# Optimization experiments

Hardware: AMD Instinct MI355X
Metric: run time of the kernel (lower is better)

## Reference

```python
import jax, jax.numpy as jnp
import numpy as np

F_DIM = 128
N_RBF = 20
CUTOFF = 5.0
N_LAYERS = 3
EPS = 1e-8


def setup_inputs() -> dict:
    key = jax.random.key(0)
    ks = jax.random.split(key, 16)
    N, E = 10000, 320000
    atomic_numbers = jax.random.randint(ks[0], (N,), 0, 100)
    r_ij = jax.random.normal(ks[1], (E, 3), dtype=jnp.float32)
    idx_i = jnp.sort(jax.random.randint(ks[2], (E,), 0, N))
    idx_j = jax.random.randint(ks[3], (E,), 0, N)
    emb = jax.random.normal(ks[4], (100, F_DIM), dtype=jnp.float32)
    emb = emb.at[0].set(0.0)  # padding_idx=0
    s = 0.05
    return {
        "atomic_numbers": atomic_numbers,
        "r_ij": r_ij,
        "idx_i": idx_i,
        "idx_j": idx_j,
        "embedding": emb,
        "filt_W": jax.random.normal(ks[5], (N_RBF, N_LAYERS * 3 * F_DIM), dtype=jnp.float32) * s,
        "filt_b": jax.random.normal(ks[6], (N_LAYERS * 3 * F_DIM,), dtype=jnp.float32) * s,
        "int_W1": jax.random.normal(ks[7], (N_LAYERS, F_DIM, F_DIM), dtype=jnp.float32) * s,
        "int_b1": jax.random.normal(ks[8], (N_LAYERS, F_DIM), dtype=jnp.float32) * s,
        "int_W2": jax.random.normal(ks[9], (N_LAYERS, F_DIM, 3 * F_DIM), dtype=jnp.float32) * s,
        "int_b2": jax.random.normal(ks[10], (N_LAYERS, 3 * F_DIM), dtype=jnp.float32) * s,
        "mix_W1": jax.random.normal(ks[11], (N_LAYERS, 2 * F_DIM, F_DIM), dtype=jnp.float32) * s,
        "mix_b1": jax.random.normal(ks[12], (N_LAYERS, F_DIM), dtype=jnp.float32) * s,
        "mix_W2": jax.random.normal(ks[13], (N_LAYERS, F_DIM, 3 * F_DIM), dtype=jnp.float32) * s,
        "mix_b2": jax.random.normal(ks[14], (N_LAYERS, 3 * F_DIM), dtype=jnp.float32) * s,
        "mux_W": jax.random.normal(ks[15], (N_LAYERS, F_DIM, 2 * F_DIM), dtype=jnp.float32) * s,
    }


def _painn(embedding, filt_W, filt_b, int_W1, int_b1, int_W2, int_b2,
           mix_W1, mix_b1, mix_W2, mix_b2, mux_W,
           r_ij, atomic_numbers, idx_i, idx_j):
    N = atomic_numbers.shape[0]
    F = F_DIM
    d_ij = jnp.linalg.norm(r_ij, axis=1, keepdims=True)          # [E,1]
    dir_ij = r_ij / d_ij                                          # [E,3]
    # Gaussian RBF expansion
    offset = jnp.linspace(0.0, CUTOFF, N_RBF, dtype=jnp.float32)
    coeff = -0.5 / (offset[1] - offset[0]) ** 2
    phi = jnp.exp(coeff * (d_ij[..., None] - offset) ** 2)        # [E,1,n_rbf]
    # Cosine cutoff
    fcut = 0.5 * (jnp.cos(d_ij * jnp.pi / CUTOFF) + 1.0) * (d_ij < CUTOFF)  # [E,1]
    filters = (phi @ filt_W + filt_b) * fcut[..., None]           # [E,1,L*3F]
    filter_list = jnp.split(filters, N_LAYERS, axis=-1)

    q = embedding[atomic_numbers][:, None, :]                     # [N,1,F]
    mu = jnp.zeros((N, 3, F), dtype=q.dtype)

    for i in range(N_LAYERS):
        Wij = filter_list[i]                                      # [E,1,3F]
        # interaction
        h = jax.nn.silu(q @ int_W1[i] + int_b1[i])
        x = h @ int_W2[i] + int_b2[i]                             # [N,1,3F]
        xj = x[idx_j]                                             # [E,1,3F]
        muj = mu[idx_j]                                           # [E,3,F]
        xw = Wij * xj
        dq, dmuR, dmumu = jnp.split(xw, 3, axis=-1)               # each [E,1,F]
        dq = jax.ops.segment_sum(dq, idx_i, num_segments=N)       # [N,1,F]
        dmu = dmuR * dir_ij[:, :, None] + dmumu * muj             # [E,3,F]
        dmu = jax.ops.segment_sum(dmu, idx_i, num_segments=N)     # [N,3,F]
        q = q + dq
        mu = mu + dmu
        # mixing
        mu_mix = mu @ mux_W[i]                                    # [N,3,2F]
        mu_V, mu_W = jnp.split(mu_mix, 2, axis=-1)
        mu_Vn = jnp.sqrt(jnp.sum(mu_V ** 2, axis=-2, keepdims=True) + EPS)  # [N,1,F]
        ctx = jnp.concatenate([q, mu_Vn], axis=-1)                # [N,1,2F]
        h = jax.nn.silu(ctx @ mix_W1[i] + mix_b1[i])
        x = h @ mix_W2[i] + mix_b2[i]                             # [N,1,3F]
        dq_i, dmu_i, dqmu_i = jnp.split(x, 3, axis=-1)
        dmu_i = dmu_i * mu_W                                      # [N,3,F]
        dqmu_i = dqmu_i * jnp.sum(mu_V * mu_W, axis=1, keepdims=True)
        q = q + dq_i + dqmu_i
        mu = mu + dmu_i
    return q[:, 0, :], mu


def reference(atomic_numbers, r_ij, idx_i, idx_j, embedding, filt_W, filt_b,
              int_W1, int_b1, int_W2, int_b2, mix_W1, mix_b1, mix_W2, mix_b2, mux_W):
    return _painn(embedding, filt_W, filt_b, int_W1, int_b1, int_W2, int_b2,
                  mix_W1, mix_b1, mix_W2, mix_b2, mux_W,
                  r_ij, atomic_numbers, idx_i, idx_j)
```

## Files before the change

kernel.cpp:

```cpp
#include <hip/hip_runtime.h>
#include <hip/hip_bf16.h>
#include <hip/hip_fp16.h>

#define F_DIM 128
#define N_RBF 20
#define CUTOFF 5.0f
#define PI_F 3.14159265358979323846f
#define NPB 4

typedef float v2f __attribute__((ext_vector_type(2)));
typedef __attribute__((ext_vector_type(8))) short bf16x8;
typedef __attribute__((ext_vector_type(4))) float f32x4;
typedef _Float16 h2f __attribute__((ext_vector_type(2)));

__device__ __forceinline__ unsigned int bf16_rtne(float f) {
    unsigned int u = __float_as_uint(f);
    u += 0x7fffu + ((u >> 16) & 1u);
    return u >> 16;
}
__device__ __forceinline__ unsigned int pack_bf2(float lo, float hi) {
    return bf16_rtne(lo) | (bf16_rtne(hi) << 16);
}
__device__ __forceinline__ float unpk_lo(unsigned int u) {
    return __uint_as_float(u << 16);
}
__device__ __forceinline__ float unpk_hi(unsigned int u) {
    return __uint_as_float(u & 0xffff0000u);
}
__device__ __forceinline__ float bf16_to_f(unsigned short s) {
    return __uint_as_float(((unsigned int)s) << 16);
}
__device__ __forceinline__ unsigned int pack_h2(float lo, float hi) {
    h2f h = (h2f){(_Float16)lo, (_Float16)hi};
    return __builtin_bit_cast(unsigned int, h);
}
__device__ __forceinline__ float fdot2f(unsigned int a, unsigned int b, float c) {
    h2f ha = __builtin_bit_cast(h2f, a);
    h2f hb = __builtin_bit_cast(h2f, b);
#if __has_builtin(__builtin_amdgcn_fdot2)
    return __builtin_amdgcn_fdot2(ha, hb, c, false);
#else
    return c + (float)ha.x * (float)hb.x + (float)ha.y * (float)hb.y;
#endif
}

__global__ __launch_bounds__(256) void k_rowptr(const int* __restrict__ idx_i,
                                                int* __restrict__ row_ptr, int N, int E) {
    int i = blockIdx.x * blockDim.x + threadIdx.x;
    if (i > N) return;
    if (i == N) { row_ptr[N] = E; return; }
    int lo = 0, hi = E;
    while (lo < hi) {
        int mid = (lo + hi) >> 1;
        if (idx_i[mid] < i) lo = mid + 1; else hi = mid;
    }
    row_ptr[i] = lo;
}

__global__ __launch_bounds__(256) void k_init(const int* __restrict__ Z,
                                              const float* __restrict__ emb,
                                              float* __restrict__ q,
                                              unsigned int* __restrict__ P,
                                              float* __restrict__ muD, int N) {
    int idx = blockIdx.x * blockDim.x + threadIdx.x;
    if (idx < N * F_DIM) {
        int n = idx >> 7, f = idx & 127;
        q[idx] = emb[Z[n] * F_DIM + f];
    }
    if (idx < N * 384) { P[idx] = 0u; muD[idx] = 0.f; }
}

__global__ __launch_bounds__(256) void k_prep(const float* __restrict__ muxW,
                                              const float* __restrict__ W1,
                                              const float* __restrict__ W2,
                                              const float* __restrict__ iW1,
                                              const float* __restrict__ iW2,
                                              const float* __restrict__ filt_W,
                                              unsigned short* __restrict__ muxWt,
                                              unsigned short* __restrict__ W1t,
                                              unsigned short* __restrict__ W2t,
                                              unsigned short* __restrict__ iW1t,
                                              unsigned short* __restrict__ iW2t,
                                              unsigned int* __restrict__ filtWh) {
    int idx = blockIdx.x * 256 + threadIdx.x;
    if (idx < 98304) {
        int l = idx / 32768, rem = idx % 32768;
        int c = rem / 128, k = rem % 128;
        muxWt[idx] = (unsigned short)bf16_rtne(muxW[l * 32768 + k * 256 + c]);
    } else if (idx < 196608) {
        int i2 = idx - 98304;
        int l = i2 / 32768, rem = i2 % 32768;
        int c = rem / 256, k = rem % 256;
        W1t[i2] = (unsigned short)bf16_rtne(W1[l * 32768 + k * 128 + c]);
    } else if (idx < 344064) {
        int i2 = idx - 196608;
        int l = i2 / 49152, rem = i2 % 49152;
        int c = rem / 128, k = rem % 128;
        W2t[i2] = (unsigned short)bf16_rtne(W2[l * 49152 + k * 384 + c]);
    } else if (idx < 393216) {
        int i2 = idx - 344064;
        int l = i2 / 16384, rem = i2 % 16384;
        int c = rem / 128, k = rem % 128;
        iW1t[i2] = (unsigned short)bf16_rtne(iW1[l * 16384 + k * 128 + c]);
    } else if (idx < 540672) {
        int i2 = idx - 393216;
        int l = i2 / 49152, rem = i2 % 49152;
        int c = rem / 128, k = rem % 128;
        iW2t[i2] = (unsigned short)bf16_rtne(iW2[l * 49152 + k * 384 + c]);
    } else if (idx < 552192) {
        int i2 = idx - 540672;
        int l = i2 / 3840, rem = i2 % 3840;
        int kp = rem / 384, c = rem % 384;
        float lo = filt_W[(2 * kp) * 1152 + l * 384 + c];
        float hi = filt_W[(2 * kp + 1) * 1152 + l * 384 + c];
        filtWh[i2] = pack_h2(lo, hi);
    }
}

__global__ __launch_bounds__(256) void k_geom(const float* __restrict__ r,
                                              unsigned int* __restrict__ geom, int E) {
    int e = blockIdx.x * blockDim.x + threadIdx.x;
    if (e >= E) return;
    float x = r[e * 3], y = r[e * 3 + 1], z = r[e * 3 + 2];
    float d = sqrtf(x * x + y * y + z * z);
    float inv = 1.f / d;
    float fc = (d < CUTOFF) ? 0.5f * (__cosf(d * (PI_F / CUTOFF)) + 1.f) : 0.f;
    unsigned int* g = geom + (size_t)e * 16;
    g[0] = __float_as_uint(x * inv);
    g[1] = __float_as_uint(y * inv);
    g[2] = __float_as_uint(z * inv);
    g[3] = __float_as_uint(fc);
    const float delta = CUTOFF / (N_RBF - 1);
    const float coeff = -0.5f / (delta * delta);
    float ph[N_RBF];
#pragma unroll
    for (int k = 0; k < N_RBF; k++) {
        float t = d - k * delta;
        ph[k] = __expf(coeff * t * t) * fc;
    }
#pragma unroll
    for (int k = 0; k < N_RBF / 2; k++)
        g[4 + k] = pack_h2(ph[2 * k], ph[2 * k + 1]);
}

__global__ __launch_bounds__(256) void k_node_mfma(
        const float* __restrict__ q,
        const unsigned short* __restrict__ iW1t,
        const float* __restrict__ b1,
        const unsigned short* __restrict__ iW2t,
        const float* __restrict__ b2,
        unsigned int* __restrict__ P, int N) {
    __shared__ unsigned short A[16 * 136];
    __shared__ unsigned short Ah[16 * 136];
    __shared__ float Xs[16 * 396];
    int t = threadIdx.x;
    int w = t >> 6, l = t & 63, quad = l >> 4, c0 = l & 15;
    int n0 = blockIdx.x * 16;

#pragma unroll
    for (int i = 0; i < 4; i++) {
        int flat = i * 256 + t;
        int node = flat >> 6, cp = flat & 63;
        int gn = n0 + node;
        unsigned int v = 0u;
        if (gn < N) { const float* s = q + (size_t)gn * 128 + 2 * cp; v = pack_bf2(s[0], s[1]); }
        *(unsigned int*)&A[node * 136 + 2 * cp] = v;
    }
    __syncthreads();

    bf16x8 a1[4];
#pragma unroll
    for (int ks = 0; ks < 4; ks++)
        a1[ks] = *(const bf16x8*)&A[c0 * 136 + ks * 32 + quad * 8];
#pragma unroll
    for (int jj = 0; jj < 2; jj++) {
        int jg = 2 * w + jj;
        float bb = b1[16 * jg + c0];
        f32x4 acc = (f32x4){bb, bb, bb, bb};
#pragma unroll
        for (int ks = 0; ks < 4; ks++) {
            bf16x8 b = *(const bf16x8*)&iW1t[(16 * jg + c0) * 128 + ks * 32 + quad * 8];
            acc = __builtin_amdgcn_mfma_f32_16x16x32_bf16(a1[ks], b, acc, 0, 0, 0);
        }
#pragma unroll
        for (int r = 0; r < 4; r++) {
            float aa = acc[r];
            Ah[(quad * 4 + r) * 136 + 16 * jg + c0] =
                (unsigned short)bf16_rtne(aa / (1.f + __expf(-aa)));
        }
    }
    __syncthreads();

    bf16x8 a3[4];
#pragma unroll
    for (int ks = 0; ks < 4; ks++)
        a3[ks] = *(const bf16x8*)&Ah[c0 * 136 + ks * 32 + quad * 8];
#pragma unroll
    for (int jj = 0; jj < 6; jj++) {
        int jx = 6 * w + jj;
        float bb = b2[16 * jx + c0];
        f32x4 acc = (f32x4){bb, bb, bb, bb};
#pragma unroll
        for (int ks = 0; ks < 4; ks++) {
            bf16x8 b = *(const bf16x8*)&iW2t[(16 * jx + c0) * 128 + ks * 32 + quad * 8];
            acc = __builtin_amdgcn_mfma_f32_16x16x32_bf16(a3[ks], b, acc, 0, 0, 0);
        }
#pragma unroll
        for (int r = 0; r < 4; r++)
            Xs[(quad * 4 + r) * 396 + 16 * jx + c0] = acc[r];
    }
    __syncthreads();

    int n = t >> 4, fi = (t & 15) * 8;
    int gn = n0 + n;
    if (gn < N) {
        size_t base = (size_t)gn * 384;
        unsigned int d[8];
#pragma unroll
        for (int k = 0; k < 8; k++) {
            float x0 = Xs[n * 396 + fi + k];
            float x1 = Xs[n * 396 + 128 + fi + k];
            float x2 = Xs[n * 396 + 256 + fi + k];
            d[k] = pack_bf2(x0, x1);
            ((unsigned short*)&P[base + 256 + fi + k])[0] = (unsigned short)bf16_rtne(x2);
        }
        *(uint4*)&P[base + fi]     = make_uint4(d[0], d[1], d[2], d[3]);
        *(uint4*)&P[base + fi + 4] = make_uint4(d[4], d[5], d[6], d[7]);
    }
}

template <bool HAS_MU>
__global__ __launch_bounds__(256) void k_edge(
        const unsigned int* __restrict__ P,
        const unsigned int* __restrict__ geom,
        const int* __restrict__ idx_j,
        const int* __restrict__ row_ptr,
        const unsigned int* __restrict__ filtWh,
        const float* __restrict__ filt_b,
        int layer,
        float* __restrict__ q,
        float* __restrict__ muD, int N) {
    __shared__ float red[4][128];
    int t = threadIdx.x;
    int f = t & 127;
    int sub = __builtin_amdgcn_readfirstlane(t >> 7);

    unsigned int Wq[N_RBF / 2], Wr[N_RBF / 2], Wm[N_RBF / 2];
    const unsigned int* Fh = filtWh + layer * 3840;
#pragma unroll
    for (int j = 0; j < N_RBF / 2; j++) {
        Wq[j] = Fh[j * 384 + f];
        Wr[j] = Fh[j * 384 + 128 + f];
        Wm[j] = Fh[j * 384 + 256 + f];
    }
    float bf0 = filt_b[layer * 384 + f];
    float bf1 = filt_b[layer * 384 + 128 + f];
    float bf2 = filt_b[layer * 384 + 256 + f];

    int i0 = blockIdx.x * NPB;
    for (int nn = 0; nn < NPB; nn++) {
        int i = i0 + nn;
        if (i >= N) break;
        int rs = __builtin_amdgcn_readfirstlane(row_ptr[i]);
        int re = __builtin_amdgcn_readfirstlane(row_ptr[i + 1]);
        float dq = 0.f;
        v2f dm01 = (v2f){0.f, 0.f};
        float dm2 = 0.f;

        for (int e = rs + sub; e < re; e += 2) {
            int j = __builtin_amdgcn_readfirstlane(idx_j[e]);
            const unsigned int* Pj = P + (size_t)j * 384;
            unsigned int A = Pj[f];
            unsigned int B = 0, C = 0;
            if (HAS_MU) { B = Pj[128 + f]; C = Pj[256 + f]; }

            const unsigned int* g = geom + (size_t)e * 16;
            float dirx = __uint_as_float(g[0]);
            float diry = __uint_as_float(g[1]);
            float dirz = __uint_as_float(g[2]);
            float fcv  = __uint_as_float(g[3]);
            unsigned int pp[10];
#pragma unroll
            for (int k = 0; k < 10; k++) pp[k] = g[4 + k];

            float wq = fcv * bf0, wr = fcv * bf1, wm = fcv * bf2;
#pragma unroll
            for (int k = 0; k < N_RBF / 2; k++) {
                wq = fdot2f(pp[k], Wq[k], wq);
                wr = fdot2f(pp[k], Wr[k], wr);
                if (HAS_MU) wm = fdot2f(pp[k], Wm[k], wm);
            }

            float xq = unpk_lo(A), xr = unpk_hi(A);
            dq += wq * xq;
            float s_r = wr * xr;
            if (HAS_MU) {
                float xm = unpk_lo(C);
                float s_m = wm * xm;
                dm01 += (v2f){s_r, s_r} * (v2f){dirx, diry} +
                        (v2f){s_m, s_m} * (v2f){unpk_lo(B), unpk_hi(B)};
                dm2  += s_r * dirz + s_m * unpk_hi(C);
            } else {
                dm01 += (v2f){s_r, s_r} * (v2f){dirx, diry};
                dm2  += s_r * dirz;
            }
        }

        if (sub == 1) { red[0][f] = dq; red[1][f] = dm01.x; red[2][f] = dm01.y; red[3][f] = dm2; }
        __syncthreads();
        if (sub == 0) {
            dq += red[0][f];
            float d0 = dm01.x + red[1][f], d1 = dm01.y + red[2][f];
            dm2 += red[3][f];
            q[(size_t)i * 128 + f] += dq;
            size_t base = (size_t)i * 384;
            if (HAS_MU) {
                muD[base + f]       += d0;
                muD[base + 128 + f] += d1;
                muD[base + 256 + f] += dm2;
            } else {
                muD[base + f]       = d0;
                muD[base + 128 + f] = d1;
                muD[base + 256 + f] = dm2;
            }
        }
        __syncthreads();
    }
}

__global__ __launch_bounds__(256) void k_mix_fused(
        float* __restrict__ q, float* __restrict__ mu,
        const unsigned short* __restrict__ muxWt,
        const unsigned short* __restrict__ W1t,
        const unsigned short* __restrict__ W2t,
        const float* __restrict__ b1,
        const float* __restrict__ b2,
        const unsigned short* __restrict__ niW1t,
        const float* __restrict__ nib1,
        const unsigned short* __restrict__ niW2t,
        const float* __restrict__ nib2,
        int has_node,
        unsigned int* __restrict__ P, int N) {
    __shared__ unsigned short A[16 * 264];
    __shared__ unsigned short Wsp[3 * 16 * 136];
    __shared__ float Xs[16 * 396];
    __shared__ float Ss[16 * 140];
    int t = threadIdx.x;
    int w = t >> 6, l = t & 63, quad = l >> 4, c0 = l & 15;
    int n0 = blockIdx.x * 16;

#pragma unroll
    for (int i = 0; i < 4; i++) {
        int flat = i * 256 + t;
        int node = flat >> 6, cp = flat & 63;
        int gn = n0 + node;
        unsigned int v = 0u;
        if (gn < N) { const float* s = q + (size_t)gn * 128 + 2 * cp; v = pack_bf2(s[0], s[1]); }
        *(unsigned int*)&A[node * 264 + 2 * cp] = v;
    }

    f32x4 vn2[2], S[2];
#pragma unroll
    for (int jj = 0; jj < 2; jj++) { vn2[jj] = (f32x4){0,0,0,0}; S[jj] = (f32x4){0,0,0,0}; }

    for (int c = 0; c < 3; c++) {
#pragma unroll
        for (int i = 0; i < 4; i++) {
            int flat = i * 256 + t;
            int node = flat >> 6, cp = flat & 63;
            int gn = n0 + node;
            unsigned int v = 0u;
            if (gn < N) {
                const float* s = mu + (size_t)gn * 384 + c * 128 + 2 * cp;
                v = pack_bf2(s[0], s[1]);
            }
            *(unsigned int*)&A[node * 264 + 128 + 2 * cp] = v;
        }
        __syncthreads();
        bf16x8 af[4];
#pragma unroll
        for (int ks = 0; ks < 4; ks++)
            af[ks] = *(const bf16x8*)&A[c0 * 264 + 128 + ks * 32 + quad * 8];
#pragma unroll
        for (int jj = 0; jj < 2; jj++) {
            int jv = 2 * w + jj;
            f32x4 V = (f32x4){0,0,0,0}, Wm = (f32x4){0,0,0,0};
#pragma unroll
            for (int ks = 0; ks < 4; ks++) {
                bf16x8 bV = *(const bf16x8*)&muxWt[(16 * jv + c0) * 128 + ks * 32 + quad * 8];
                V = __builtin_amdgcn_mfma_f32_16x16x32_bf16(af[ks], bV, V, 0, 0, 0);
            }
#pragma unroll
            for (int ks = 0; ks < 4; ks++) {
                bf16x8 bW = *(const bf16x8*)&muxWt[(16 * (jv + 8) + c0) * 128 + ks * 32 + quad * 8];
                Wm = __builtin_amdgcn_mfma_f32_16x16x32_bf16(af[ks], bW, Wm, 0, 0, 0);
            }
            vn2[jj] += V * V;
            S[jj]   += V * Wm;
#pragma unroll
            for (int r = 0; r < 4; r++)
                Wsp[c * 2176 + (quad * 4 + r) * 136 + 16 * jv + c0] =
                    (unsigned short)bf16_rtne(Wm[r]);
        }
        __syncthreads();
    }

#pragma unroll
    for (int jj = 0; jj < 2; jj++) {
        int jv = 2 * w + jj;
#pragma unroll
        for (int r = 0; r < 4; r++)
            A[(quad * 4 + r) * 264 + 128 + 16 * jv + c0] =
                (unsigned short)bf16_rtne(sqrtf(vn2[jj][r] + 1e-8f));
    }
    __syncthreads();

    bf16x8 a2[8];
#pragma unroll
    for (int ks = 0; ks < 8; ks++)
        a2[ks] = *(const bf16x8*)&A[c0 * 264 + ks * 32 + quad * 8];
    {
        unsigned short htmp[2][4];
#pragma unroll
        for (int jj = 0; jj < 2; jj++) {
            int jg = 2 * w + jj;
            float bb = b1[16 * jg + c0];
            f32x4 acc = (f32x4){bb, bb, bb, bb};
#pragma unroll
            for (int ks = 0; ks < 8; ks++) {
                bf16x8 b = *(const bf16x8*)&W1t[(16 * jg + c0) * 256 + ks * 32 + quad * 8];
                acc = __builtin_amdgcn_mfma_f32_16x16x32_bf16(a2[ks], b, acc, 0, 0, 0);
            }
#pragma unroll
            for (int r = 0; r < 4; r++) {
                float aa = acc[r];
                htmp[jj][r] = (unsigned short)bf16_rtne(aa / (1.f + __expf(-aa)));
            }
        }
        __syncthreads();
#pragma unroll
        for (int jj = 0; jj < 2; jj++) {
            int jg = 2 * w + jj;
#pragma unroll
            for (int r = 0; r < 4; r++)
                A[(quad * 4 + r) * 264 + 128 + 16 * jg + c0] = htmp[jj][r];
        }
    }
    __syncthreads();

    bf16x8 a3[4];
#pragma unroll
    for (int ks = 0; ks < 4; ks++)
        a3[ks] = *(const bf16x8*)&A[c0 * 264 + 128 + ks * 32 + quad * 8];
#pragma unroll
    for (int jj = 0; jj < 6; jj++) {
        int jx = 6 * w + jj;
        float bb = b2[16 * jx + c0];
        f32x4 acc = (f32x4){bb, bb, bb, bb};
#pragma unroll
        for (int ks = 0; ks < 4; ks++) {
            bf16x8 b = *(const bf16x8*)&W2t[(16 * jx + c0) * 128 + ks * 32 + quad * 8];
            acc = __builtin_amdgcn_mfma_f32_16x16x32_bf16(a3[ks], b, acc, 0, 0, 0);
        }
#pragma unroll
        for (int r = 0; r < 4; r++)
            Xs[(quad * 4 + r) * 396 + 16 * jx + c0] = acc[r];
    }
#pragma unroll
    for (int jj = 0; jj < 2; jj++) {
        int jv = 2 * w + jj;
#pragma unroll
        for (int r = 0; r < 4; r++)
            Ss[(quad * 4 + r) * 140 + 16 * jv + c0] = S[jj][r];
    }
    __syncthreads();

    int n = t >> 4, fi = (t & 15) * 8;
    int gn = n0 + n;
    if (gn < N) {
        float* qp = q + (size_t)gn * 128 + fi;
        float qn[8];
#pragma unroll
        for (int k = 0; k < 8; k++) {
            qn[k] = qp[k] + Xs[n * 396 + fi + k] +
                    Xs[n * 396 + 256 + fi + k] * Ss[n * 140 + fi + k];
            qp[k] = qn[k];
        }
        unsigned int qd[4];
#pragma unroll
        for (int p = 0; p < 4; p++) qd[p] = pack_bf2(qn[2 * p], qn[2 * p + 1]);
        *(uint4*)&A[n * 264 + fi] = make_uint4(qd[0], qd[1], qd[2], qd[3]);

        size_t base = (size_t)gn * 384;
        float m[3][8];
#pragma unroll
        for (int c = 0; c < 3; c++) {
            float* mp = mu + base + c * 128 + fi;
#pragma unroll
            for (int k = 0; k < 8; k++) {
                m[c][k] = mp[k] + Xs[n * 396 + 128 + fi + k] *
                                  bf16_to_f(Wsp[c * 2176 + n * 136 + fi + k]);
                mp[k] = m[c][k];
            }
        }
        unsigned int d[8];
#pragma unroll
        for (int k = 0; k < 8; k++) {
            d[k] = pack_bf2(m[0][k], m[1][k]);
            ((unsigned short*)&P[base + 256 + fi + k])[1] = (unsigned short)bf16_rtne(m[2][k]);
        }
        *(uint4*)&P[base + 128 + fi]     = make_uint4(d[0], d[1], d[2], d[3]);
        *(uint4*)&P[base + 128 + fi + 4] = make_uint4(d[4], d[5], d[6], d[7]);
    }
    __syncthreads();

    if (has_node) {
        unsigned short* Ah = Wsp;
        bf16x8 a1[4];
#pragma unroll
        for (int ks = 0; ks < 4; ks++)
            a1[ks] = *(const bf16x8*)&A[c0 * 264 + ks * 32 + quad * 8];
#pragma unroll
        for (int jj = 0; jj < 2; jj++) {
            int jg = 2 * w + jj;
            float bb = nib1[16 * jg + c0];
            f32x4 acc = (f32x4){bb, bb, bb, bb};
#pragma unroll
            for (int ks = 0; ks < 4; ks++) {
                bf16x8 b = *(const bf16x8*)&niW1t[(16 * jg + c0) * 128 + ks * 32 + quad * 8];
                acc = __builtin_amdgcn_mfma_f32_16x16x32_bf16(a1[ks], b, acc, 0, 0, 0);
            }
#pragma unroll
            for (int r = 0; r < 4; r++) {
                float aa = acc[r];
                Ah[(quad * 4 + r) * 136 + 16 * jg + c0] =
                    (unsigned short)bf16_rtne(aa / (1.f + __expf(-aa)));
            }
        }
        __syncthreads();

        bf16x8 a4[4];
#pragma unroll
        for (int ks = 0; ks < 4; ks++)
            a4[ks] = *(const bf16x8*)&Ah[c0 * 136 + ks * 32 + quad * 8];
#pragma unroll
        for (int jj = 0; jj < 6; jj++) {
            int jx = 6 * w + jj;
            float bb = nib2[16 * jx + c0];
            f32x4 acc = (f32x4){bb, bb, bb, bb};
#pragma unroll
            for (int ks = 0; ks < 4; ks++) {
                bf16x8 b = *(const bf16x8*)&niW2t[(16 * jx + c0) * 128 + ks * 32 + quad * 8];
                acc = __builtin_amdgcn_mfma_f32_16x16x32_bf16(a4[ks], b, acc, 0, 0, 0);
            }
#pragma unroll
            for (int r = 0; r < 4; r++)
                Xs[(quad * 4 + r) * 396 + 16 * jx + c0] = acc[r];
        }
        __syncthreads();

        if (gn < N) {
            size_t base = (size_t)gn * 384;
            unsigned int d[8];
#pragma unroll
            for (int k = 0; k < 8; k++) {
                float x0 = Xs[n * 396 + fi + k];
                float x1 = Xs[n * 396 + 128 + fi + k];
                float x2 = Xs[n * 396 + 256 + fi + k];
                d[k] = pack_bf2(x0, x1);
                ((unsigned short*)&P[base + 256 + fi + k])[0] = (unsigned short)bf16_rtne(x2);
            }
            *(uint4*)&P[base + fi]     = make_uint4(d[0], d[1], d[2], d[3]);
            *(uint4*)&P[base + fi + 4] = make_uint4(d[4], d[5], d[6], d[7]);
        }
    }
}

extern "C" void kernel_launch(void* const* d_in, const int* in_sizes, int n_in,
                              void* d_out, int out_size, void* d_ws, size_t ws_size,
                              hipStream_t stream) {
    const int*   Z      = (const int*)d_in[0];
    const float* r_ij   = (const float*)d_in[1];
    const int*   idx_i  = (const int*)d_in[2];
    const int*   idx_j  = (const int*)d_in[3];
    const float* emb    = (const float*)d_in[4];
    const float* filt_W = (const float*)d_in[5];
    const float* filt_b = (const float*)d_in[6];
    const float* int_W1 = (const float*)d_in[7];
    const float* int_b1 = (const float*)d_in[8];
    const float* int_W2 = (const float*)d_in[9];
    const float* int_b2 = (const float*)d_in[10];
    const float* mix_W1 = (const float*)d_in[11];
    const float* mix_b1 = (const float*)d_in[12];
    const float* mix_W2 = (const float*)d_in[13];
    const float* mix_b2 = (const float*)d_in[14];
    const float* mux_W  = (const float*)d_in[15];

    int N = in_sizes[0];
    int E = in_sizes[2];

    float* q   = (float*)d_out;
    float* muD = q + (size_t)N * 128;

    unsigned int* geom = (unsigned int*)d_ws;
    unsigned int* P = geom + (size_t)E * 16;
    int* row_ptr = (int*)(P + (size_t)N * 384);
    uintptr_t waddr = (uintptr_t)(row_ptr + N + 1);
    waddr = (waddr + 15) & ~(uintptr_t)15;
    unsigned short* muxWt = (unsigned short*)waddr;
    unsigned short* W1t   = muxWt + 98304;
    unsigned short* W2t   = W1t + 98304;
    unsigned short* iW1t  = W2t + 147456;
    unsigned short* iW2t  = iW1t + 49152;
    unsigned int* filtWh  = (unsigned int*)(iW2t + 147456);

    k_rowptr<<<(N + 1 + 255) / 256, 256, 0, stream>>>(idx_i, row_ptr, N, E);
    k_init<<<((size_t)N * 384 + 255) / 256, 256, 0, stream>>>(Z, emb, q, P, muD, N);
    k_geom<<<(E + 255) / 256, 256, 0, stream>>>(r_ij, geom, E);
    k_prep<<<2157, 256, 0, stream>>>(mux_W, mix_W1, mix_W2, int_W1, int_W2, filt_W,
                                     muxWt, W1t, W2t, iW1t, iW2t, filtWh);

    int tiles = (N + 15) / 16;
    k_node_mfma<<<tiles, 256, 0, stream>>>(
        q, iW1t, int_b1, iW2t, int_b2, P, N);
    for (int l = 0; l < 3; l++) {
        if (l == 0)
            k_edge<false><<<(N + NPB - 1) / NPB, 256, 0, stream>>>(
                P, geom, idx_j, row_ptr, filtWh, filt_b, l, q, muD, N);
        else
            k_edge<true><<<(N + NPB - 1) / NPB, 256, 0, stream>>>(
                P, geom, idx_j, row_ptr, filtWh, filt_b, l, q, muD, N);
        int nl = (l < 2) ? (l + 1) : 0;
        k_mix_fused<<<tiles, 256, 0, stream>>>(
            q, muD, muxWt + (size_t)l * 32768, W1t + (size_t)l * 32768,
            W2t + (size_t)l * 49152, mix_b1 + l * 128, mix_b2 + l * 384,
            iW1t + (size_t)nl * 16384, int_b1 + nl * 128,
            iW2t + (size_t)nl * 49152, int_b2 + nl * 384,
            (l < 2) ? 1 : 0, P, N);
    }
}
```

Baseline: 543.2 us.

## Compute edge filter weights with fp16 MFMA tiles staged through shared memory

Replaces the per-thread fdot2 RBF-to-filter projection in the edge kernel with 16x16x32 fp16 MFMA over tiles of 16 edges. The bias is folded in as an extra K column multiplied by fc. Filter weights are re-laid out in prep as K-padded fp16 B fragments, and the resulting per-edge weights go into an LDS buffer that the gather loop then reads. This cuts redundant ALU work, since the old code recomputed each edge's filter per feature lane. In exchange it adds two block syncs per 16-edge tile, and rows have only about 32 edges, so padded tiles waste work.

```diff
diff --git a/kernel.cpp b/kernel.cpp
--- a/kernel.cpp
+++ b/kernel.cpp
@@ -12,6 +12,7 @@
 typedef __attribute__((ext_vector_type(8))) short bf16x8;
 typedef __attribute__((ext_vector_type(4))) float f32x4;
 typedef _Float16 h2f __attribute__((ext_vector_type(2)));
+typedef _Float16 f16x8 __attribute__((ext_vector_type(8)));
 
 __device__ __forceinline__ unsigned int bf16_rtne(float f) {
     unsigned int u = __float_as_uint(f);
@@ -33,15 +34,6 @@
 __device__ __forceinline__ unsigned int pack_h2(float lo, float hi) {
     h2f h = (h2f){(_Float16)lo, (_Float16)hi};
     return __builtin_bit_cast(unsigned int, h);
-}
-__device__ __forceinline__ float fdot2f(unsigned int a, unsigned int b, float c) {
-    h2f ha = __builtin_bit_cast(h2f, a);
-    h2f hb = __builtin_bit_cast(h2f, b);
-#if __has_builtin(__builtin_amdgcn_fdot2)
-    return __builtin_amdgcn_fdot2(ha, hb, c, false);
-#else
-    return c + (float)ha.x * (float)hb.x + (float)ha.y * (float)hb.y;
-#endif
 }
 
 __global__ __launch_bounds__(256) void k_rowptr(const int* __restrict__ idx_i,
@@ -76,12 +68,13 @@
                                               const float* __restrict__ iW1,
                                               const float* __restrict__ iW2,
                                               const float* __restrict__ filt_W,
+                                              const float* __restrict__ filt_b,
                                               unsigned short* __restrict__ muxWt,
                                               unsigned short* __restrict__ W1t,
                                               unsigned short* __restrict__ W2t,
                                               unsigned short* __restrict__ iW1t,
                                               unsigned short* __restrict__ iW2t,
-                                              unsigned int* __restrict__ filtWh) {
+                                              unsigned short* __restrict__ filtWt) {
     int idx = blockIdx.x * 256 + threadIdx.x;
     if (idx < 98304) {
         int l = idx / 32768, rem = idx % 32768;
@@ -107,13 +100,15 @@
         int l = i2 / 49152, rem = i2 % 49152;
         int c = rem / 128, k = rem % 128;
         iW2t[i2] = (unsigned short)bf16_rtne(iW2[l * 49152 + k * 384 + c]);
-    } else if (idx < 552192) {
+    } else if (idx < 568320) {
         int i2 = idx - 540672;
-        int l = i2 / 3840, rem = i2 % 3840;
-        int kp = rem / 384, c = rem % 384;
-        float lo = filt_W[(2 * kp) * 1152 + l * 384 + c];
-        float hi = filt_W[(2 * kp + 1) * 1152 + l * 384 + c];
-        filtWh[i2] = pack_h2(lo, hi);
+        int l = i2 / 9216, rem = i2 % 9216;
+        int c = rem / 24, k = rem % 24;
+        float v = 0.f;
+        if (k < 20)       v = filt_W[k * 1152 + l * 384 + c];
+        else if (k == 20) v = filt_b[l * 384 + c];
+        _Float16 hv = (_Float16)v;
+        filtWt[i2] = __builtin_bit_cast(unsigned short, hv);
     }
 }
 
@@ -141,6 +136,8 @@
 #pragma unroll
     for (int k = 0; k < N_RBF / 2; k++)
         g[4 + k] = pack_h2(ph[2 * k], ph[2 * k + 1]);
+    g[14] = pack_h2(fc, 0.f);
+    g[15] = 0u;
 }
 
 __global__ __launch_bounds__(256) void k_node_mfma(
@@ -229,33 +226,43 @@
     }
 }
 
+__device__ __forceinline__ f16x8 load_phi_frag(const unsigned int* __restrict__ geom,
+                                               int ts, int c0, int quad, int E) {
+    int ea = ts + c0;
+    if (ea >= E) ea = E - 1;
+    f16x8 a = {};
+    if (quad < 3)
+        a = *(const f16x8*)&geom[(size_t)ea * 16 + 4 + quad * 4];
+    return a;
+}
+
 template <bool HAS_MU>
 __global__ __launch_bounds__(256) void k_edge(
         const unsigned int* __restrict__ P,
         const unsigned int* __restrict__ geom,
         const int* __restrict__ idx_j,
         const int* __restrict__ row_ptr,
-        const unsigned int* __restrict__ filtWh,
-        const float* __restrict__ filt_b,
-        int layer,
+        const unsigned short* __restrict__ filtWt,
         float* __restrict__ q,
-        float* __restrict__ muD, int N) {
+        float* __restrict__ muD, int N, int E) {
+    constexpr int NT = HAS_MU ? 6 : 4;
+    constexpr int WS = 388;
+    __shared__ float Ws[16 * WS];
     __shared__ float red[4][128];
     int t = threadIdx.x;
     int f = t & 127;
     int sub = __builtin_amdgcn_readfirstlane(t >> 7);
-
-    unsigned int Wq[N_RBF / 2], Wr[N_RBF / 2], Wm[N_RBF / 2];
-    const unsigned int* Fh = filtWh + layer * 3840;
-#pragma unroll
-    for (int j = 0; j < N_RBF / 2; j++) {
-        Wq[j] = Fh[j * 384 + f];
-        Wr[j] = Fh[j * 384 + 128 + f];
-        Wm[j] = Fh[j * 384 + 256 + f];
-    }
-    float bf0 = filt_b[layer * 384 + f];
-    float bf1 = filt_b[layer * 384 + 128 + f];
-    float bf2 = filt_b[layer * 384 + 256 + f];
+    int w = t >> 6, l = t & 63, quad = l >> 4, c0 = l & 15;
+
+    f16x8 Bf[NT];
+#pragma unroll
+    for (int jj = 0; jj < NT; jj++) {
+        int jx = NT * w + jj;
+        f16x8 b = {};
+        if (quad < 3)
+            b = *(const f16x8*)&filtWt[(16 * jx + c0) * 24 + quad * 8];
+        Bf[jj] = b;
+    }
 
     int i0 = blockIdx.x * NPB;
     for (int nn = 0; nn < NPB; nn++) {
@@ -267,43 +274,51 @@
         v2f dm01 = (v2f){0.f, 0.f};
         float dm2 = 0.f;
 
-        for (int e = rs + sub; e < re; e += 2) {
-            int j = __builtin_amdgcn_readfirstlane(idx_j[e]);
-            const unsigned int* Pj = P + (size_t)j * 384;
-            unsigned int A = Pj[f];
-            unsigned int B = 0, C = 0;
-            if (HAS_MU) { B = Pj[128 + f]; C = Pj[256 + f]; }
-
-            const unsigned int* g = geom + (size_t)e * 16;
-            float dirx = __uint_as_float(g[0]);
-            float diry = __uint_as_float(g[1]);
-            float dirz = __uint_as_float(g[2]);
-            float fcv  = __uint_as_float(g[3]);
-            unsigned int pp[10];
-#pragma unroll
-            for (int k = 0; k < 10; k++) pp[k] = g[4 + k];
-
-            float wq = fcv * bf0, wr = fcv * bf1, wm = fcv * bf2;
-#pragma unroll
-            for (int k = 0; k < N_RBF / 2; k++) {
-                wq = fdot2f(pp[k], Wq[k], wq);
-                wr = fdot2f(pp[k], Wr[k], wr);
-                if (HAS_MU) wm = fdot2f(pp[k], Wm[k], wm);
-            }
-
-            float xq = unpk_lo(A), xr = unpk_hi(A);
-            dq += wq * xq;
-            float s_r = wr * xr;
-            if (HAS_MU) {
-                float xm = unpk_lo(C);
-                float s_m = wm * xm;
-                dm01 += (v2f){s_r, s_r} * (v2f){dirx, diry} +
-                        (v2f){s_m, s_m} * (v2f){unpk_lo(B), unpk_hi(B)};
-                dm2  += s_r * dirz + s_m * unpk_hi(C);
-            } else {
-                dm01 += (v2f){s_r, s_r} * (v2f){dirx, diry};
-                dm2  += s_r * dirz;
-            }
+        f16x8 a = load_phi_frag(geom, rs, c0, quad, E);
+        for (int ts = rs; ts < re; ts += 16) {
+#pragma unroll
+            for (int jj = 0; jj < NT; jj++) {
+                int jx = NT * w + jj;
+                f32x4 acc = (f32x4){0.f, 0.f, 0.f, 0.f};
+                acc = __builtin_amdgcn_mfma_f32_16x16x32_f16(a, Bf[jj], acc, 0, 0, 0);
+#pragma unroll
+                for (int r = 0; r < 4; r++)
+                    Ws[(quad * 4 + r) * WS + 16 * jx + c0] = acc[r];
+            }
+            __syncthreads();
+            if (ts + 16 < re) a = load_phi_frag(geom, ts + 16, c0, quad, E);
+
+            int te = (re < ts + 16) ? re : ts + 16;
+            for (int e = ts + sub; e < te; e += 2) {
+                int j = __builtin_amdgcn_readfirstlane(idx_j[e]);
+                const unsigned int* Pj = P + (size_t)j * 384;
+                unsigned int A = Pj[f];
+                unsigned int B = 0, C = 0;
+                if (HAS_MU) { B = Pj[128 + f]; C = Pj[256 + f]; }
+
+                const float* g = (const float*)(geom + (size_t)e * 16);
+                float dirx = g[0], diry = g[1], dirz = g[2];
+
+                int eloc = e - ts;
+                float wq = Ws[eloc * WS + f];
+                float wr = Ws[eloc * WS + 128 + f];
+
+                float xq = unpk_lo(A), xr = unpk_hi(A);
+                dq += wq * xq;
+                float s_r = wr * xr;
+                if (HAS_MU) {
+                    float wm = Ws[eloc * WS + 256 + f];
+                    float xm = unpk_lo(C);
+                    float s_m = wm * xm;
+                    dm01 += (v2f){s_r, s_r} * (v2f){dirx, diry} +
+                            (v2f){s_m, s_m} * (v2f){unpk_lo(B), unpk_hi(B)};
+                    dm2  += s_r * dirz + s_m * unpk_hi(C);
+                } else {
+                    dm01 += (v2f){s_r, s_r} * (v2f){dirx, diry};
+                    dm2  += s_r * dirz;
+                }
+            }
+            __syncthreads();
         }
 
         if (sub == 1) { red[0][f] = dq; red[1][f] = dm01.x; red[2][f] = dm01.y; red[3][f] = dm2; }
@@ -612,13 +627,13 @@
     unsigned short* W2t   = W1t + 98304;
     unsigned short* iW1t  = W2t + 147456;
     unsigned short* iW2t  = iW1t + 49152;
-    unsigned int* filtWh  = (unsigned int*)(iW2t + 147456);
+    unsigned short* filtWt = iW2t + 147456;
 
     k_rowptr<<<(N + 1 + 255) / 256, 256, 0, stream>>>(idx_i, row_ptr, N, E);
     k_init<<<((size_t)N * 384 + 255) / 256, 256, 0, stream>>>(Z, emb, q, P, muD, N);
     k_geom<<<(E + 255) / 256, 256, 0, stream>>>(r_ij, geom, E);
-    k_prep<<<2157, 256, 0, stream>>>(mux_W, mix_W1, mix_W2, int_W1, int_W2, filt_W,
-                                     muxWt, W1t, W2t, iW1t, iW2t, filtWh);
+    k_prep<<<2220, 256, 0, stream>>>(mux_W, mix_W1, mix_W2, int_W1, int_W2, filt_W, filt_b,
+                                     muxWt, W1t, W2t, iW1t, iW2t, filtWt);
 
     int tiles = (N + 15) / 16;
     k_node_mfma<<<tiles, 256, 0, stream>>>(
@@ -626,10 +641,10 @@
     for (int l = 0; l < 3; l++) {
         if (l == 0)
             k_edge<false><<<(N + NPB - 1) / NPB, 256, 0, stream>>>(
-                P, geom, idx_j, row_ptr, filtWh, filt_b, l, q, muD, N);
+                P, geom, idx_j, row_ptr, filtWt, q, muD, N, E);
         else
             k_edge<true><<<(N + NPB - 1) / NPB, 256, 0, stream>>>(
-                P, geom, idx_j, row_ptr, filtWh, filt_b, l, q, muD, N);
+                P, geom, idx_j, row_ptr, filtWt + (size_t)l * 9216, q, muD, N, E);
         int nl = (l < 2) ? (l + 1) : 0;
         k_mix_fused<<<tiles, 256, 0, stream>>>(
             q, muD, muxWt + (size_t)l * 32768, W1t + (size_t)l * 32768,
```

New measurement: 539.9 us. No clear change (-0.6%).
